# Kernel optimization log

Measured on AMD Instinct MI355X. Metric: run time of the kernel, lower is better.

The kernel has to match this reference:

```python
import jax, jax.numpy as jnp
import numpy as np
import math

L_LAYERS = 4
D = 768
H = 12
HD = D // H
S = 2048
BATCH = 1
V = 32000
R = 32
DFF = 3072
LORA_SCALE = 1.0 / R
EPS = 1e-6
NEG_INF = -1e9


def _alibi_slopes(n):
    def pow2(m):
        start = 2 ** (-2 ** (-(math.log2(m) - 3)))
        ratio = 2 ** (1.0 / m)
        return [start / ratio ** i for i in range(m)]
    if n <= 8:
        return [2 ** (-8.0 / n * (i + 1)) for i in range(n)]
    if math.log2(n).is_integer():
        return pow2(n)
    cp = 2 ** round(math.log2(n))
    base = pow2(cp)
    if n > cp:
        extra = []
        for _ in range(n - cp):
            r = base[-1] / base[-2] if len(base) > 1 else 0.5
            extra.append(base[-1] * r)
        return base + extra
    return base[:n]


def setup_inputs() -> dict:
    key = jax.random.key(0)
    ks = iter(jax.random.split(key, 24))
    def w(shape):
        return jax.random.normal(next(ks), shape, dtype=jnp.float32) * 0.02
    return {
        'input_ids': jax.random.randint(next(ks), (BATCH, S), 0, V),
        'emb': w((V, D)),
        'slopes': jnp.array(_alibi_slopes(H), dtype=jnp.float32),
        'ln1_g': jnp.ones((L_LAYERS, D), jnp.float32),
        'ln1_b': jnp.zeros((L_LAYERS, D), jnp.float32),
        'qkv_W': w((L_LAYERS, 3 * D, D)),
        'qkv_A': w((L_LAYERS, D, R)),
        'qkv_B': w((L_LAYERS, R, 3 * D)),
        'out_W': w((L_LAYERS, D, D)),
        'out_A': w((L_LAYERS, D, R)),
        'out_B': w((L_LAYERS, R, D)),
        'ln2_g': jnp.ones((L_LAYERS, D), jnp.float32),
        'ln2_b': jnp.zeros((L_LAYERS, D), jnp.float32),
        'fc1_W': w((L_LAYERS, 2 * DFF, D)),
        'fc1_A': w((L_LAYERS, D, R)),
        'fc1_B': w((L_LAYERS, R, 2 * DFF)),
        'fc2_W': w((L_LAYERS, D, DFF)),
        'fc2_A': w((L_LAYERS, DFF, R)),
        'fc2_B': w((L_LAYERS, R, D)),
        'ls1': 0.1 * jnp.ones((L_LAYERS, D), jnp.float32),
        'ls2': 0.1 * jnp.ones((L_LAYERS, D), jnp.float32),
        'lnf_g': jnp.ones((D,), jnp.float32),
        'lnf_b': jnp.zeros((D,), jnp.float32),
    }


def _ln(x, g, b):
    m = x.mean(-1, keepdims=True)
    v = jnp.mean((x - m) ** 2, -1, keepdims=True)
    return (x - m) * jax.lax.rsqrt(v + EPS) * g + b


def _lora(x, W, A, B):
    # base nn.Linear (weight [out,in], no bias) + low-rank adaptation
    return x @ W.T + (x @ A) @ B * LORA_SCALE


def _forward(input_ids, emb, slopes, ln1_g, ln1_b, qkv_W, qkv_A, qkv_B,
             out_W, out_A, out_B, ln2_g, ln2_b, fc1_W, fc1_A, fc1_B,
             fc2_W, fc2_A, fc2_B, ls1, ls2, lnf_g, lnf_b):
    bsz, s = input_ids.shape
    n_heads = slopes.shape[0]
    hd = emb.shape[1] // n_heads
    d = emb.shape[1]
    x = emb[input_ids]  # [B,S,D]

    # ALiBi bias + causal mask: [H,S,S]
    pos = jnp.arange(s)
    rel = pos[None, :] - pos[:, None]  # j - i, <= 0 in causal region
    bias = jnp.where(rel <= 0, slopes[:, None, None] * rel, NEG_INF)

    scale = 1.0 / math.sqrt(hd)
    n_layers = qkv_W.shape[0]
    for l in range(n_layers):
        # --- attention block ---
        h = _ln(x, ln1_g[l], ln1_b[l])
        qkv = _lora(h, qkv_W[l], qkv_A[l], qkv_B[l])  # [B,S,3D]
        qkv = qkv.reshape(bsz, s, 3, n_heads, hd)
        q = qkv[:, :, 0].transpose(0, 2, 1, 3)  # [B,H,S,hd]
        k = qkv[:, :, 1].transpose(0, 2, 1, 3)
        v = qkv[:, :, 2].transpose(0, 2, 1, 3)
        scores = jnp.einsum('bhid,bhjd->bhij', q, k) * scale + bias[None]
        wts = jax.nn.softmax(scores, axis=-1)
        ao = jnp.einsum('bhij,bhjd->bhid', wts, v)
        ao = ao.transpose(0, 2, 1, 3).reshape(bsz, s, d)
        ao = _lora(ao, out_W[l], out_A[l], out_B[l])
        x = x + ls1[l] * ao  # LayerScale, dropout=identity (eval)

        # --- SwiGLU FFN block ---
        h = _ln(x, ln2_g[l], ln2_b[l])
        hidden = _lora(h, fc1_W[l], fc1_A[l], fc1_B[l])  # [B,S,2*DFF]
        gated, activated = jnp.split(hidden, 2, axis=-1)
        ff = jax.nn.silu(gated) * activated
        ff = _lora(ff, fc2_W[l], fc2_A[l], fc2_B[l])
        x = x + ls2[l] * ff

    x = _ln(x, lnf_g, lnf_b)
    logits = x @ emb.T  # tied lm_head
    return logits


def reference(input_ids, emb, slopes, ln1_g, ln1_b, qkv_W, qkv_A, qkv_B,
              out_W, out_A, out_B, ln2_g, ln2_b, fc1_W, fc1_A, fc1_B,
              fc2_W, fc2_A, fc2_B, ls1, ls2, lnf_g, lnf_b):
    return _forward(input_ids, emb, slopes, ln1_g, ln1_b, qkv_W, qkv_A, qkv_B,
                    out_W, out_A, out_B, ln2_g, ln2_b, fc1_W, fc1_A, fc1_B,
                    fc2_W, fc2_A, fc2_B, ls1, ls2, lnf_g, lnf_b)
```

## Files before the change

kernel.cpp:

```cpp
#include <hip/hip_runtime.h>
#include <hip/hip_bf16.h>
#include <stdint.h>

#define S 2048
#define D 768
#define H 12
#define HD 64
#define V 32000
#define R 32
#define DFF 3072
#define NLAYERS 4
#define EPS 1e-6f

typedef __bf16 bf16;
typedef __bf16 bf16x4 __attribute__((ext_vector_type(4)));
typedef __bf16 bf16x8 __attribute__((ext_vector_type(8)));
typedef float f32x4 __attribute__((ext_vector_type(4)));

__device__ __forceinline__ int swz_logical(int nwg) {
    int id = blockIdx.x;
    int q = nwg >> 3;
    return (id & 7) * q + (id >> 3);
}

__global__ __launch_bounds__(256) void k_cvt(const float* __restrict__ in,
                                             bf16* __restrict__ out, long n) {
    long i = ((long)blockIdx.x * 256 + threadIdx.x) * 4;
    if (i >= n) return;
    float4 v = *(const float4*)(in + i);
    bf16x4 o;
    o.x = (bf16)v.x; o.y = (bf16)v.y; o.z = (bf16)v.z; o.w = (bf16)v.w;
    *(bf16x4*)(out + i) = o;
}

__global__ __launch_bounds__(256) void k_fold(const float* __restrict__ W,
                                              const float* __restrict__ A,
                                              const float* __restrict__ B,
                                              bf16* __restrict__ Wb,
                                              int N, int K) {
    __shared__ float As[256][33];
    int l = blockIdx.z;
    const float* Wl = W + (long)l * N * K;
    const float* Al = A + (long)l * K * R;
    const float* Bl = B + (long)l * R * N;
    bf16* Wbl = Wb + (long)l * N * K;
    int t = threadIdx.x;
    long k0 = (long)blockIdx.x * 256;
    int n0 = blockIdx.y * 8;
    const float* Ab = Al + k0 * R;
    #pragma unroll
    for (int i = 0; i < 32; ++i) {
        int idx = i * 256 + t;
        As[idx >> 5][idx & 31] = Ab[idx];
    }
    __syncthreads();
    long k = k0 + t;
    float acc[8];
    #pragma unroll
    for (int j = 0; j < 8; ++j) acc[j] = Wl[(long)(n0 + j) * K + k];
    for (int r = 0; r < R; ++r) {
        float a = As[t][r] * (1.0f / R);
        #pragma unroll
        for (int j = 0; j < 8; ++j)
            acc[j] = fmaf(a, Bl[(long)r * N + n0 + j], acc[j]);
    }
    #pragma unroll
    for (int j = 0; j < 8; ++j) Wbl[(long)(n0 + j) * K + k] = (bf16)acc[j];
}

__global__ void k_embed(const int* __restrict__ ids, const float* __restrict__ emb,
                        float* __restrict__ x) {
    int s = blockIdx.x;
    int row = ids[s];
    for (int d = threadIdx.x; d < D; d += blockDim.x)
        x[s * D + d] = emb[row * D + d];
}

__global__ __launch_bounds__(256) void k_ln_bf(const float* __restrict__ x,
                                               const float* __restrict__ g,
                                               const float* __restrict__ b,
                                               bf16* __restrict__ out) {
    int w = threadIdx.x >> 6, lane = threadIdx.x & 63;
    long s = (long)blockIdx.x * 4 + w;
    const float* xr = x + s * D;
    float4 v0 = *(const float4*)(xr + lane * 4);
    float4 v1 = *(const float4*)(xr + 256 + lane * 4);
    float4 v2 = *(const float4*)(xr + 512 + lane * 4);
    float sum = v0.x + v0.y + v0.z + v0.w + v1.x + v1.y + v1.z + v1.w
              + v2.x + v2.y + v2.z + v2.w;
    float sq = v0.x*v0.x + v0.y*v0.y + v0.z*v0.z + v0.w*v0.w
             + v1.x*v1.x + v1.y*v1.y + v1.z*v1.z + v1.w*v1.w
             + v2.x*v2.x + v2.y*v2.y + v2.z*v2.z + v2.w*v2.w;
    #pragma unroll
    for (int m = 1; m < 64; m <<= 1) {
        sum += __shfl_xor(sum, m);
        sq  += __shfl_xor(sq, m);
    }
    float mean = sum * (1.0f / D);
    float var  = sq * (1.0f / D) - mean * mean;
    float rs = rsqrtf(var + EPS);
    bf16* orow = out + s * D;
    #pragma unroll
    for (int j = 0; j < 3; ++j) {
        float4 v = (j == 0) ? v0 : (j == 1) ? v1 : v2;
        float4 gv = *(const float4*)(g + j * 256 + lane * 4);
        float4 bv = *(const float4*)(b + j * 256 + lane * 4);
        bf16x4 o;
        o[0] = (bf16)((v.x - mean) * rs * gv.x + bv.x);
        o[1] = (bf16)((v.y - mean) * rs * gv.y + bv.y);
        o[2] = (bf16)((v.z - mean) * rs * gv.z + bv.z);
        o[3] = (bf16)((v.w - mean) * rs * gv.w + bv.w);
        *(bf16x4*)(orow + j * 256 + lane * 4) = o;
    }
}

__device__ __forceinline__ void gload16(const bf16* g, bf16* l) {
    __builtin_amdgcn_global_load_lds(
        (const __attribute__((address_space(1))) void*)g,
        (__attribute__((address_space(3))) void*)l, 16, 0, 0);
}

__global__ __launch_bounds__(256) void k_gemm_lm(const bf16* __restrict__ X,
                                                 const bf16* __restrict__ W,
                                                 float* __restrict__ C,
                                                 int N, int K, int nwg) {
    __shared__ bf16 At[128 * 32];
    __shared__ bf16 Bt[128 * 32];
    int tid = threadIdx.x;
    int w = tid >> 6, lane = tid & 63;
    int logical = swz_logical(nwg);
    long m0 = (long)(logical & 15) * 128;
    long n0 = (long)(logical >> 4) * 128;
    int wr = (w >> 1) * 64, wc = (w & 1) * 64;
    int c0 = w, c1 = w + 4;
    int rA0 = c0 * 16 + (lane >> 2);
    int rA1 = c1 * 16 + (lane >> 2);
    int ck = (lane & 3) * 8;
    int fr = lane & 15;
    int fo = (lane >> 4) * 8;
    f32x4 acc[4][4] = {};
    for (int k0 = 0; k0 < K; k0 += 32) {
        gload16(X + (m0 + rA0) * K + k0 + ck, At + c0 * 512);
        gload16(X + (m0 + rA1) * K + k0 + ck, At + c1 * 512);
        gload16(W + (n0 + rA0) * K + k0 + ck, Bt + c0 * 512);
        gload16(W + (n0 + rA1) * K + k0 + ck, Bt + c1 * 512);
        __syncthreads();
        bf16x8 a[4], b[4];
        #pragma unroll
        for (int m = 0; m < 4; m++)
            a[m] = *(const bf16x8*)(At + (wr + m * 16 + fr) * 32 + fo);
        #pragma unroll
        for (int n = 0; n < 4; n++)
            b[n] = *(const bf16x8*)(Bt + (wc + n * 16 + fr) * 32 + fo);
        #pragma unroll
        for (int m = 0; m < 4; m++)
            #pragma unroll
            for (int n = 0; n < 4; n++)
                acc[m][n] = __builtin_amdgcn_mfma_f32_16x16x32_bf16(a[m], b[n], acc[m][n], 0, 0, 0);
        __syncthreads();
    }
    int cr = (lane >> 4) * 4, cc = lane & 15;
    #pragma unroll
    for (int m = 0; m < 4; m++)
        #pragma unroll
        for (int n = 0; n < 4; n++) {
            long col = n0 + wc + n * 16 + cc;
            #pragma unroll
            for (int r = 0; r < 4; r++) {
                long idx = (m0 + wr + m * 16 + cr + r) * N + col;
                C[idx] = acc[m][n][r];
            }
        }
}

template <int TAG>
__global__ __launch_bounds__(256) void k_gemm_small(const bf16* __restrict__ X,
                                                    const bf16* __restrict__ W,
                                                    float* __restrict__ C,
                                                    int N, int K,
                                                    const float* __restrict__ ls,
                                                    int nwg) {
    __shared__ bf16 At[64 * 64];
    __shared__ bf16 Bt[128 * 64];
    int tid = threadIdx.x;
    int w = tid >> 6, lane = tid & 63;
    int logical = swz_logical(nwg);
    long m0 = (long)(logical & 31) * 64;
    long n0 = (long)(logical >> 5) * 128;
    int wr = (w >> 1) * 32, wc = (w & 1) * 64;
    int fr = lane & 15;
    int g  = lane >> 4;
    f32x4 acc[2][4] = {};
    for (int k0 = 0; k0 < K; k0 += 64) {
        #pragma unroll
        for (int i = 0; i < 2; ++i) {
            int ci = tid + 256 * i;
            int r = ci >> 3, c = (ci & 7) ^ (r & 7);
            gload16(X + (m0 + r) * K + k0 + c * 8, At + ci * 8);
        }
        #pragma unroll
        for (int i = 0; i < 4; ++i) {
            int ci = tid + 256 * i;
            int r = ci >> 3, c = (ci & 7) ^ (r & 7);
            gload16(W + (n0 + r) * K + k0 + c * 8, Bt + ci * 8);
        }
        __syncthreads();
        #pragma unroll
        for (int kk = 0; kk < 2; ++kk) {
            bf16x8 a[2], b[4];
            #pragma unroll
            for (int m = 0; m < 2; m++) {
                int row = wr + m * 16 + fr;
                a[m] = *(const bf16x8*)(At + row * 64 + (((kk * 4 + g) ^ (row & 7)) * 8));
            }
            #pragma unroll
            for (int n = 0; n < 4; n++) {
                int row = wc + n * 16 + fr;
                b[n] = *(const bf16x8*)(Bt + row * 64 + (((kk * 4 + g) ^ (row & 7)) * 8));
            }
            #pragma unroll
            for (int m = 0; m < 2; m++)
                #pragma unroll
                for (int n = 0; n < 4; n++)
                    acc[m][n] = __builtin_amdgcn_mfma_f32_16x16x32_bf16(a[m], b[n], acc[m][n], 0, 0, 0);
        }
        __syncthreads();
    }
    int cr = (lane >> 4) * 4, cc = lane & 15;
    #pragma unroll
    for (int m = 0; m < 2; m++)
        #pragma unroll
        for (int n = 0; n < 4; n++) {
            long col = n0 + wc + n * 16 + cc;
            #pragma unroll
            for (int r = 0; r < 4; r++) {
                long idx = (m0 + wr + m * 16 + cr + r) * N + col;
                C[idx] = fmaf(ls[col], acc[m][n][r], C[idx]);
            }
        }
}

__global__ __launch_bounds__(256) void k_gemm_qkv(const bf16* __restrict__ X,
                                                  const bf16* __restrict__ W,
                                                  bf16* __restrict__ Qh,
                                                  bf16* __restrict__ Kh,
                                                  bf16* __restrict__ Vt,
                                                  int nwg) {
    const int K = D;
    __shared__ bf16 smem[128 * 136];
    bf16* At = smem;
    bf16* Bt = smem + 128 * 32;
    int tid = threadIdx.x;
    int w = tid >> 6, lane = tid & 63;
    int logical = swz_logical(nwg);
    long m0 = (long)(logical & 15) * 128;
    long n0 = (long)(logical >> 4) * 128;
    int wr = (w >> 1) * 64, wc = (w & 1) * 64;
    int c0 = w, c1 = w + 4;
    int rA0 = c0 * 16 + (lane >> 2);
    int rA1 = c1 * 16 + (lane >> 2);
    int ck = (lane & 3) * 8;
    int fr = lane & 15;
    int fo = (lane >> 4) * 8;
    f32x4 acc[4][4] = {};
    for (int k0 = 0; k0 < K; k0 += 32) {
        gload16(X + (m0 + rA0) * K + k0 + ck, At + c0 * 512);
        gload16(X + (m0 + rA1) * K + k0 + ck, At + c1 * 512);
        gload16(W + (n0 + rA0) * K + k0 + ck, Bt + c0 * 512);
        gload16(W + (n0 + rA1) * K + k0 + ck, Bt + c1 * 512);
        __syncthreads();
        bf16x8 a[4], b[4];
        #pragma unroll
        for (int m = 0; m < 4; m++)
            a[m] = *(const bf16x8*)(At + (wr + m * 16 + fr) * 32 + fo);
        #pragma unroll
        for (int n = 0; n < 4; n++)
            b[n] = *(const bf16x8*)(Bt + (wc + n * 16 + fr) * 32 + fo);
        #pragma unroll
        for (int m = 0; m < 4; m++)
            #pragma unroll
            for (int n = 0; n < 4; n++)
                acc[m][n] = __builtin_amdgcn_mfma_f32_16x16x32_bf16(a[m], b[n], acc[m][n], 0, 0, 0);
        __syncthreads();
    }
    int cr = (lane >> 4) * 4, cc = lane & 15;
    if (n0 < 1536) {
        float scale = (n0 < 768) ? 0.125f : 1.0f;
        bf16* dst = (n0 < 768) ? Qh : Kh;
        int base = (n0 < 768) ? (int)n0 : (int)n0 - 768;
        #pragma unroll
        for (int m = 0; m < 4; m++)
            #pragma unroll
            for (int n = 0; n < 4; n++)
                #pragma unroll
                for (int r = 0; r < 4; r++)
                    smem[(wr + m * 16 + cr + r) * 136 + wc + n * 16 + cc] =
                        (bf16)(acc[m][n][r] * scale);
        __syncthreads();
        #pragma unroll
        for (int i = 0; i < 8; ++i) {
            int c = tid + 256 * i;
            int srow = c >> 4, off = (c & 15) * 8;
            int hh = (base >> 6) + (off >> 6);
            int d0 = off & 63;
            bf16x8 vv = *(const bf16x8*)(smem + srow * 136 + off);
            *(bf16x8*)(dst + ((long)hh * S + m0 + srow) * HD + d0) = vv;
        }
    } else {
        int base = (int)n0 - 1536;
        #pragma unroll
        for (int m = 0; m < 4; m++)
            #pragma unroll
            for (int n = 0; n < 4; n++) {
                bf16x4 pv;
                #pragma unroll
                for (int r = 0; r < 4; ++r) pv[r] = (bf16)acc[m][n][r];
                *(bf16x4*)(smem + (wc + n * 16 + cc) * 136 + wr + m * 16 + cr) = pv;
            }
        __syncthreads();
        #pragma unroll
        for (int i = 0; i < 8; ++i) {
            int c = tid + 256 * i;
            int vcol = c >> 4, soff = (c & 15) * 8;
            bf16x8 vv = *(const bf16x8*)(smem + vcol * 136 + soff);
            *(bf16x8*)(Vt + (long)(base + vcol) * S + m0 + soff) = vv;
        }
    }
}

__global__ __launch_bounds__(256) void k_gemm_fc1(const bf16* __restrict__ X,
                                                  const bf16* __restrict__ W,
                                                  bf16* __restrict__ hb,
                                                  int nwg) {
    const int K = D;
    __shared__ bf16 At[128 * 32];
    __shared__ bf16 Bg[128 * 32];
    __shared__ bf16 Ba[128 * 32];
    int tid = threadIdx.x;
    int w = tid >> 6, lane = tid & 63;
    int logical = swz_logical(nwg);
    long m0 = (long)(logical & 15) * 128;
    long f0 = (long)(logical >> 4) * 128;
    int wr = (w >> 1) * 64, wc = (w & 1) * 64;
    int c0 = w, c1 = w + 4;
    int rA0 = c0 * 16 + (lane >> 2);
    int rA1 = c1 * 16 + (lane >> 2);
    int ck = (lane & 3) * 8;
    int fr = lane & 15;
    int fo = (lane >> 4) * 8;
    const bf16* Wg = W + f0 * K;
    const bf16* Wa = W + ((long)DFF + f0) * K;
    f32x4 accG[4][4] = {}, accA[4][4] = {};
    for (int k0 = 0; k0 < K; k0 += 32) {
        gload16(X + (m0 + rA0) * K + k0 + ck, At + c0 * 512);
        gload16(X + (m0 + rA1) * K + k0 + ck, At + c1 * 512);
        gload16(Wg + (long)rA0 * K + k0 + ck, Bg + c0 * 512);
        gload16(Wg + (long)rA1 * K + k0 + ck, Bg + c1 * 512);
        gload16(Wa + (long)rA0 * K + k0 + ck, Ba + c0 * 512);
        gload16(Wa + (long)rA1 * K + k0 + ck, Ba + c1 * 512);
        __syncthreads();
        bf16x8 a[4], bg[4], ba[4];
        #pragma unroll
        for (int m = 0; m < 4; m++)
            a[m] = *(const bf16x8*)(At + (wr + m * 16 + fr) * 32 + fo);
        #pragma unroll
        for (int n = 0; n < 4; n++) {
            bg[n] = *(const bf16x8*)(Bg + (wc + n * 16 + fr) * 32 + fo);
            ba[n] = *(const bf16x8*)(Ba + (wc + n * 16 + fr) * 32 + fo);
        }
        #pragma unroll
        for (int m = 0; m < 4; m++)
            #pragma unroll
            for (int n = 0; n < 4; n++) {
                accG[m][n] = __builtin_amdgcn_mfma_f32_16x16x32_bf16(a[m], bg[n], accG[m][n], 0, 0, 0);
                accA[m][n] = __builtin_amdgcn_mfma_f32_16x16x32_bf16(a[m], ba[n], accA[m][n], 0, 0, 0);
            }
        __syncthreads();
    }
    int cr = (lane >> 4) * 4, cc = lane & 15;
    #pragma unroll
    for (int m = 0; m < 4; m++)
        #pragma unroll
        for (int n = 0; n < 4; n++) {
            long col = f0 + wc + n * 16 + cc;
            #pragma unroll
            for (int r = 0; r < 4; r++) {
                long s = m0 + wr + m * 16 + cr + r;
                float gv = accG[m][n][r], av = accA[m][n][r];
                float sig = 1.0f / (1.0f + __expf(-gv));
                hb[s * DFF + col] = (bf16)(gv * sig * av);
            }
        }
}

__global__ __launch_bounds__(256) void k_attn_mfma(const bf16* __restrict__ Qh,
                                                   const bf16* __restrict__ Kh,
                                                   const bf16* __restrict__ Vt,
                                                   const float* __restrict__ slopes,
                                                   bf16* __restrict__ ao) {
    __shared__ bf16 Kl[128 * 64];
    __shared__ bf16 Vl[64 * 128];
    __shared__ bf16 Pl[4][16 * 136];
    int tid = threadIdx.x;
    int w = tid >> 6, lane = tid & 63;
    int fr = lane & 15, g = lane >> 4;
    int qb = gridDim.x - 1 - blockIdx.x;
    int q0 = qb * 64;
    int h = blockIdx.y;
    int ntiles = qb / 2 + 1;
    float slope = slopes[h];

    const bf16* qrow = Qh + ((long)h * S + q0 + w * 16 + fr) * HD;
    bf16x8 qf0 = *(const bf16x8*)(qrow + g * 8);
    bf16x8 qf1 = *(const bf16x8*)(qrow + 32 + g * 8);

    const bf16* Kg = Kh + (long)h * S * HD;
    const bf16* Vg = Vt + (long)h * HD * S;

    float m = -1e9f, l = 0.f;
    f32x4 o[4] = {};
    int qg = q0 + w * 16 + fr;

    for (int t = 0; t < ntiles; ++t) {
        int j0 = t * 128;
        __syncthreads();
        #pragma unroll
        for (int i = 0; i < 4; ++i) {
            int ci = tid + 256 * i;
            int r = ci >> 3, c = (ci & 7) ^ (r & 7);
            gload16(Kg + (long)(j0 + r) * HD + c * 8, Kl + ci * 8);
        }
        #pragma unroll
        for (int i = 0; i < 4; ++i) {
            int ci = tid + 256 * i;
            int rd = ci >> 4, cj = (ci & 15) ^ (rd & 7);
            gload16(Vg + (long)rd * S + j0 + cj * 8, Vl + ci * 8);
        }
        __syncthreads();

        f32x4 sc[8];
        __builtin_amdgcn_s_setprio(1);
        #pragma unroll
        for (int jt = 0; jt < 8; ++jt) {
            int jr = jt * 16 + fr;
            bf16x8 kf0 = *(const bf16x8*)(Kl + jr * 64 + ((g ^ (jr & 7)) * 8));
            bf16x8 kf1 = *(const bf16x8*)(Kl + jr * 64 + (((g + 4) ^ (jr & 7)) * 8));
            f32x4 z = {};
            z = __builtin_amdgcn_mfma_f32_16x16x32_bf16(kf0, qf0, z, 0, 0, 0);
            z = __builtin_amdgcn_mfma_f32_16x16x32_bf16(kf1, qf1, z, 0, 0, 0);
            sc[jt] = z;
        }
        __builtin_amdgcn_s_setprio(0);

        bool need_mask = (j0 + 127) > (q0 + w * 16);
        float mt = -1e9f;
        if (need_mask) {
            #pragma unroll
            for (int jt = 0; jt < 8; ++jt)
                #pragma unroll
                for (int r = 0; r < 4; ++r) {
                    int rel = (j0 + jt * 16 + g * 4 + r) - qg;
                    float v = (rel <= 0) ? fmaf(slope, (float)rel, sc[jt][r]) : -1e9f;
                    sc[jt][r] = v;
                    mt = fmaxf(mt, v);
                }
        } else {
            #pragma unroll
            for (int jt = 0; jt < 8; ++jt)
                #pragma unroll
                for (int r = 0; r < 4; ++r) {
                    int rel = (j0 + jt * 16 + g * 4 + r) - qg;
                    float v = fmaf(slope, (float)rel, sc[jt][r]);
                    sc[jt][r] = v;
                    mt = fmaxf(mt, v);
                }
        }
        mt = fmaxf(mt, __shfl_xor(mt, 16));
        mt = fmaxf(mt, __shfl_xor(mt, 32));
        float mnew = fmaxf(m, mt);
        float factor = __expf(m - mnew);
        float psum = 0.f;
        #pragma unroll
        for (int jt = 0; jt < 8; ++jt) {
            bf16x4 pb;
            #pragma unroll
            for (int r = 0; r < 4; ++r) {
                float p = __expf(sc[jt][r] - mnew);
                psum += p;
                pb[r] = (bf16)p;
            }
            *(bf16x4*)(&Pl[w][fr * 136 + jt * 16 + g * 4]) = pb;
        }
        psum += __shfl_xor(psum, 16);
        psum += __shfl_xor(psum, 32);
        l = l * factor + psum;
        m = mnew;
        #pragma unroll
        for (int dt = 0; dt < 4; ++dt)
            #pragma unroll
            for (int r = 0; r < 4; ++r) o[dt][r] *= factor;

        bf16x8 pf[4];
        #pragma unroll
        for (int ks = 0; ks < 4; ++ks)
            pf[ks] = *(const bf16x8*)(&Pl[w][fr * 136 + ks * 32 + g * 8]);
        __builtin_amdgcn_s_setprio(1);
        #pragma unroll
        for (int dt = 0; dt < 4; ++dt) {
            int dr = dt * 16 + fr;
            #pragma unroll
            for (int ks = 0; ks < 4; ++ks) {
                bf16x8 vf = *(const bf16x8*)(Vl + dr * 128 + (((ks * 4 + g) ^ (dr & 7)) * 8));
                o[dt] = __builtin_amdgcn_mfma_f32_16x16x32_bf16(vf, pf[ks], o[dt], 0, 0, 0);
            }
        }
        __builtin_amdgcn_s_setprio(0);
    }
    float inv = 1.0f / l;
    bf16* orow = ao + ((long)(q0 + w * 16 + fr)) * D + h * HD;
    #pragma unroll
    for (int dt = 0; dt < 4; ++dt) {
        bf16x4 ob;
        #pragma unroll
        for (int r = 0; r < 4; ++r) ob[r] = (bf16)(o[dt][r] * inv);
        *(bf16x4*)(orow + dt * 16 + g * 4) = ob;
    }
}

extern "C" void kernel_launch(void* const* d_in, const int* in_sizes, int n_in,
                              void* d_out, int out_size, void* d_ws, size_t ws_size,
                              hipStream_t stream) {
    const int*   ids    = (const int*)d_in[0];
    const float* emb    = (const float*)d_in[1];
    const float* slopes = (const float*)d_in[2];
    const float* ln1_g  = (const float*)d_in[3];
    const float* ln1_b  = (const float*)d_in[4];
    const float* qkv_W  = (const float*)d_in[5];
    const float* qkv_A  = (const float*)d_in[6];
    const float* qkv_B  = (const float*)d_in[7];
    const float* out_W  = (const float*)d_in[8];
    const float* out_A  = (const float*)d_in[9];
    const float* out_B  = (const float*)d_in[10];
    const float* ln2_g  = (const float*)d_in[11];
    const float* ln2_b  = (const float*)d_in[12];
    const float* fc1_W  = (const float*)d_in[13];
    const float* fc1_A  = (const float*)d_in[14];
    const float* fc1_B  = (const float*)d_in[15];
    const float* fc2_W  = (const float*)d_in[16];
    const float* fc2_A  = (const float*)d_in[17];
    const float* fc2_B  = (const float*)d_in[18];
    const float* ls1    = (const float*)d_in[19];
    const float* ls2    = (const float*)d_in[20];
    const float* lnf_g  = (const float*)d_in[21];
    const float* lnf_b  = (const float*)d_in[22];

    char* p = (char*)d_ws;
    float* x      = (float*)p;               p += (long)S * D * 4;
    bf16* h_bf    = (bf16*)p;                p += (long)S * D * 2;
    bf16* ao_bf   = (bf16*)p;                p += (long)S * D * 2;
    bf16* hid_bf  = (bf16*)p;                p += (long)S * DFF * 2;
    bf16* Qh      = (bf16*)p;                p += (long)H * S * HD * 2;
    bf16* Kh      = (bf16*)p;                p += (long)H * S * HD * 2;
    bf16* Vt      = (bf16*)p;                p += (long)H * HD * S * 2;
    bf16* emb_bf  = (bf16*)p;                p += (long)V * D * 2;
    bf16* qkvW_bf = (bf16*)p;                p += (long)NLAYERS * 3 * D * D * 2;
    bf16* outW_bf = (bf16*)p;                p += (long)NLAYERS * D * D * 2;
    bf16* fc1W_bf = (bf16*)p;                p += (long)NLAYERS * 2 * DFF * D * 2;
    bf16* fc2W_bf = (bf16*)p;                p += (long)NLAYERS * D * DFF * 2;

    k_fold<<<dim3(D / 256, 3 * D / 8, NLAYERS), 256, 0, stream>>>(qkv_W, qkv_A, qkv_B, qkvW_bf, 3 * D, D);
    k_fold<<<dim3(D / 256, D / 8, NLAYERS), 256, 0, stream>>>(out_W, out_A, out_B, outW_bf, D, D);
    k_fold<<<dim3(D / 256, 2 * DFF / 8, NLAYERS), 256, 0, stream>>>(fc1_W, fc1_A, fc1_B, fc1W_bf, 2 * DFF, D);
    k_fold<<<dim3(DFF / 256, D / 8, NLAYERS), 256, 0, stream>>>(fc2_W, fc2_A, fc2_B, fc2W_bf, D, DFF);
    {
        long n = (long)V * D;
        k_cvt<<<(n / 4 + 255) / 256, 256, 0, stream>>>(emb, emb_bf, n);
    }

    k_embed<<<S, 256, 0, stream>>>(ids, emb, x);

    const int NWG_QKV = (3 * D / 128) * 16;
    const int NWG_FC1 = (DFF / 128) * 16;
    const int NWG_SM  = (S / 64) * (D / 128);
    const int NWG_LM  = (V / 128) * 16;

    for (int l = 0; l < NLAYERS; l++) {
        k_ln_bf<<<S / 4, 256, 0, stream>>>(x, ln1_g + l * D, ln1_b + l * D, h_bf);
        k_gemm_qkv<<<NWG_QKV, 256, 0, stream>>>(h_bf, qkvW_bf + (long)l * 3 * D * D, Qh, Kh, Vt, NWG_QKV);
        k_attn_mfma<<<dim3(S / 64, H), 256, 0, stream>>>(Qh, Kh, Vt, slopes, ao_bf);
        k_gemm_small<1><<<NWG_SM, 256, 0, stream>>>(ao_bf, outW_bf + (long)l * D * D, x, D, D, ls1 + l * D, NWG_SM);

        k_ln_bf<<<S / 4, 256, 0, stream>>>(x, ln2_g + l * D, ln2_b + l * D, h_bf);
        k_gemm_fc1<<<NWG_FC1, 256, 0, stream>>>(h_bf, fc1W_bf + (long)l * 2 * DFF * D, hid_bf, NWG_FC1);
        k_gemm_small<2><<<NWG_SM, 256, 0, stream>>>(hid_bf, fc2W_bf + (long)l * D * DFF, x, D, DFF, ls2 + l * D, NWG_SM);
    }

    k_ln_bf<<<S / 4, 256, 0, stream>>>(x, lnf_g, lnf_b, h_bf);
    k_gemm_lm<<<NWG_LM, 256, 0, stream>>>(h_bf, emb_bf, (float*)d_out, V, D, NWG_LM);
}
```

Measured before the change: 1.230 ms.

## Retile QKV and FC1 GEMMs to 64x128 tiles with K=64 and XOR-swizzled LDS

The QKV and fused FC1 SwiGLU GEMMs switch from 128x128 tiles with K-step 32 to 64x128 tiles with K-step 64. Shared-memory tiles now use an XOR swizzle on 16-byte chunks to avoid bank conflicts. Launch grids double accordingly, giving more workgroups and fewer syncs per K loop, to improve occupancy and wave coverage across CUs. The trade-off is less A/B reuse per tile and more redundant weight loads, plus the V-transpose epilogue now uses a narrower staging stride.

```diff
diff --git a/kernel.cpp b/kernel.cpp
--- a/kernel.cpp
+++ b/kernel.cpp
@@ -247,40 +247,51 @@
                                                   bf16* __restrict__ Vt,
                                                   int nwg) {
     const int K = D;
-    __shared__ bf16 smem[128 * 136];
+    __shared__ bf16 smem[64 * 64 + 128 * 64];
     bf16* At = smem;
-    bf16* Bt = smem + 128 * 32;
+    bf16* Bt = smem + 64 * 64;
     int tid = threadIdx.x;
     int w = tid >> 6, lane = tid & 63;
     int logical = swz_logical(nwg);
-    long m0 = (long)(logical & 15) * 128;
-    long n0 = (long)(logical >> 4) * 128;
-    int wr = (w >> 1) * 64, wc = (w & 1) * 64;
-    int c0 = w, c1 = w + 4;
-    int rA0 = c0 * 16 + (lane >> 2);
-    int rA1 = c1 * 16 + (lane >> 2);
-    int ck = (lane & 3) * 8;
+    long m0 = (long)(logical & 31) * 64;
+    long n0 = (long)(logical >> 5) * 128;
+    int wr = (w >> 1) * 32, wc = (w & 1) * 64;
     int fr = lane & 15;
-    int fo = (lane >> 4) * 8;
-    f32x4 acc[4][4] = {};
-    for (int k0 = 0; k0 < K; k0 += 32) {
-        gload16(X + (m0 + rA0) * K + k0 + ck, At + c0 * 512);
-        gload16(X + (m0 + rA1) * K + k0 + ck, At + c1 * 512);
-        gload16(W + (n0 + rA0) * K + k0 + ck, Bt + c0 * 512);
-        gload16(W + (n0 + rA1) * K + k0 + ck, Bt + c1 * 512);
-        __syncthreads();
-        bf16x8 a[4], b[4];
-        #pragma unroll
-        for (int m = 0; m < 4; m++)
-            a[m] = *(const bf16x8*)(At + (wr + m * 16 + fr) * 32 + fo);
-        #pragma unroll
-        for (int n = 0; n < 4; n++)
-            b[n] = *(const bf16x8*)(Bt + (wc + n * 16 + fr) * 32 + fo);
-        #pragma unroll
-        for (int m = 0; m < 4; m++)
-            #pragma unroll
-            for (int n = 0; n < 4; n++)
-                acc[m][n] = __builtin_amdgcn_mfma_f32_16x16x32_bf16(a[m], b[n], acc[m][n], 0, 0, 0);
+    int g  = lane >> 4;
+    f32x4 acc[2][4] = {};
+    for (int k0 = 0; k0 < K; k0 += 64) {
+        #pragma unroll
+        for (int i = 0; i < 2; ++i) {
+            int ci = tid + 256 * i;
+            int r = ci >> 3, c = (ci & 7) ^ (r & 7);
+            gload16(X + (m0 + r) * K + k0 + c * 8, At + ci * 8);
+        }
+        #pragma unroll
+        for (int i = 0; i < 4; ++i) {
+            int ci = tid + 256 * i;
+            int r = ci >> 3, c = (ci & 7) ^ (r & 7);
+            gload16(W + (n0 + r) * K + k0 + c * 8, Bt + ci * 8);
+        }
+        __syncthreads();
+        #pragma unroll
+        for (int kk = 0; kk < 2; ++kk) {
+            bf16x8 a[2], b[4];
+            #pragma unroll
+            for (int m = 0; m < 2; m++) {
+                int row = wr + m * 16 + fr;
+                a[m] = *(const bf16x8*)(At + row * 64 + (((kk * 4 + g) ^ (row & 7)) * 8));
+            }
+            #pragma unroll
+            for (int n = 0; n < 4; n++) {
+                int row = wc + n * 16 + fr;
+                b[n] = *(const bf16x8*)(Bt + row * 64 + (((kk * 4 + g) ^ (row & 7)) * 8));
+            }
+            #pragma unroll
+            for (int m = 0; m < 2; m++)
+                #pragma unroll
+                for (int n = 0; n < 4; n++)
+                    acc[m][n] = __builtin_amdgcn_mfma_f32_16x16x32_bf16(a[m], b[n], acc[m][n], 0, 0, 0);
+        }
         __syncthreads();
     }
     int cr = (lane >> 4) * 4, cc = lane & 15;
@@ -289,7 +300,7 @@
         bf16* dst = (n0 < 768) ? Qh : Kh;
         int base = (n0 < 768) ? (int)n0 : (int)n0 - 768;
         #pragma unroll
-        for (int m = 0; m < 4; m++)
+        for (int m = 0; m < 2; m++)
             #pragma unroll
             for (int n = 0; n < 4; n++)
                 #pragma unroll
@@ -298,7 +309,7 @@
                         (bf16)(acc[m][n][r] * scale);
         __syncthreads();
         #pragma unroll
-        for (int i = 0; i < 8; ++i) {
+        for (int i = 0; i < 4; ++i) {
             int c = tid + 256 * i;
             int srow = c >> 4, off = (c & 15) * 8;
             int hh = (base >> 6) + (off >> 6);
@@ -309,20 +320,20 @@
     } else {
         int base = (int)n0 - 1536;
         #pragma unroll
-        for (int m = 0; m < 4; m++)
+        for (int m = 0; m < 2; m++)
             #pragma unroll
             for (int n = 0; n < 4; n++) {
                 bf16x4 pv;
                 #pragma unroll
                 for (int r = 0; r < 4; ++r) pv[r] = (bf16)acc[m][n][r];
-                *(bf16x4*)(smem + (wc + n * 16 + cc) * 136 + wr + m * 16 + cr) = pv;
-            }
-        __syncthreads();
-        #pragma unroll
-        for (int i = 0; i < 8; ++i) {
+                *(bf16x4*)(smem + (wc + n * 16 + cc) * 72 + wr + m * 16 + cr) = pv;
+            }
+        __syncthreads();
+        #pragma unroll
+        for (int i = 0; i < 4; ++i) {
             int c = tid + 256 * i;
-            int vcol = c >> 4, soff = (c & 15) * 8;
-            bf16x8 vv = *(const bf16x8*)(smem + vcol * 136 + soff);
+            int vcol = c >> 3, soff = (c & 7) * 8;
+            bf16x8 vv = *(const bf16x8*)(smem + vcol * 72 + soff);
             *(bf16x8*)(Vt + (long)(base + vcol) * S + m0 + soff) = vv;
         }
     }
@@ -333,53 +344,63 @@
                                                   bf16* __restrict__ hb,
                                                   int nwg) {
     const int K = D;
-    __shared__ bf16 At[128 * 32];
-    __shared__ bf16 Bg[128 * 32];
-    __shared__ bf16 Ba[128 * 32];
+    __shared__ bf16 At[64 * 64];
+    __shared__ bf16 Bg[128 * 64];
+    __shared__ bf16 Ba[128 * 64];
     int tid = threadIdx.x;
     int w = tid >> 6, lane = tid & 63;
     int logical = swz_logical(nwg);
-    long m0 = (long)(logical & 15) * 128;
-    long f0 = (long)(logical >> 4) * 128;
-    int wr = (w >> 1) * 64, wc = (w & 1) * 64;
-    int c0 = w, c1 = w + 4;
-    int rA0 = c0 * 16 + (lane >> 2);
-    int rA1 = c1 * 16 + (lane >> 2);
-    int ck = (lane & 3) * 8;
+    long m0 = (long)(logical & 31) * 64;
+    long f0 = (long)(logical >> 5) * 128;
+    int wr = (w >> 1) * 32, wc = (w & 1) * 64;
     int fr = lane & 15;
-    int fo = (lane >> 4) * 8;
+    int g  = lane >> 4;
     const bf16* Wg = W + f0 * K;
     const bf16* Wa = W + ((long)DFF + f0) * K;
-    f32x4 accG[4][4] = {}, accA[4][4] = {};
-    for (int k0 = 0; k0 < K; k0 += 32) {
-        gload16(X + (m0 + rA0) * K + k0 + ck, At + c0 * 512);
-        gload16(X + (m0 + rA1) * K + k0 + ck, At + c1 * 512);
-        gload16(Wg + (long)rA0 * K + k0 + ck, Bg + c0 * 512);
-        gload16(Wg + (long)rA1 * K + k0 + ck, Bg + c1 * 512);
-        gload16(Wa + (long)rA0 * K + k0 + ck, Ba + c0 * 512);
-        gload16(Wa + (long)rA1 * K + k0 + ck, Ba + c1 * 512);
-        __syncthreads();
-        bf16x8 a[4], bg[4], ba[4];
-        #pragma unroll
-        for (int m = 0; m < 4; m++)
-            a[m] = *(const bf16x8*)(At + (wr + m * 16 + fr) * 32 + fo);
-        #pragma unroll
-        for (int n = 0; n < 4; n++) {
-            bg[n] = *(const bf16x8*)(Bg + (wc + n * 16 + fr) * 32 + fo);
-            ba[n] = *(const bf16x8*)(Ba + (wc + n * 16 + fr) * 32 + fo);
-        }
-        #pragma unroll
-        for (int m = 0; m < 4; m++)
+    f32x4 accG[2][4] = {}, accA[2][4] = {};
+    for (int k0 = 0; k0 < K; k0 += 64) {
+        #pragma unroll
+        for (int i = 0; i < 2; ++i) {
+            int ci = tid + 256 * i;
+            int r = ci >> 3, c = (ci & 7) ^ (r & 7);
+            gload16(X + (m0 + r) * K + k0 + c * 8, At + ci * 8);
+        }
+        #pragma unroll
+        for (int i = 0; i < 4; ++i) {
+            int ci = tid + 256 * i;
+            int r = ci >> 3, c = (ci & 7) ^ (r & 7);
+            gload16(Wg + (long)r * K + k0 + c * 8, Bg + ci * 8);
+            gload16(Wa + (long)r * K + k0 + c * 8, Ba + ci * 8);
+        }
+        __syncthreads();
+        #pragma unroll
+        for (int kk = 0; kk < 2; ++kk) {
+            bf16x8 a[2], bg[4], ba[4];
+            #pragma unroll
+            for (int m = 0; m < 2; m++) {
+                int row = wr + m * 16 + fr;
+                a[m] = *(const bf16x8*)(At + row * 64 + (((kk * 4 + g) ^ (row & 7)) * 8));
+            }
             #pragma unroll
             for (int n = 0; n < 4; n++) {
-                accG[m][n] = __builtin_amdgcn_mfma_f32_16x16x32_bf16(a[m], bg[n], accG[m][n], 0, 0, 0);
-                accA[m][n] = __builtin_amdgcn_mfma_f32_16x16x32_bf16(a[m], ba[n], accA[m][n], 0, 0, 0);
-            }
+                int row = wc + n * 16 + fr;
+                int off = row * 64 + (((kk * 4 + g) ^ (row & 7)) * 8);
+                bg[n] = *(const bf16x8*)(Bg + off);
+                ba[n] = *(const bf16x8*)(Ba + off);
+            }
+            #pragma unroll
+            for (int m = 0; m < 2; m++)
+                #pragma unroll
+                for (int n = 0; n < 4; n++) {
+                    accG[m][n] = __builtin_amdgcn_mfma_f32_16x16x32_bf16(a[m], bg[n], accG[m][n], 0, 0, 0);
+                    accA[m][n] = __builtin_amdgcn_mfma_f32_16x16x32_bf16(a[m], ba[n], accA[m][n], 0, 0, 0);
+                }
+        }
         __syncthreads();
     }
     int cr = (lane >> 4) * 4, cc = lane & 15;
     #pragma unroll
-    for (int m = 0; m < 4; m++)
+    for (int m = 0; m < 2; m++)
         #pragma unroll
         for (int n = 0; n < 4; n++) {
             long col = f0 + wc + n * 16 + cc;
@@ -579,8 +600,8 @@
 
     k_embed<<<S, 256, 0, stream>>>(ids, emb, x);
 
-    const int NWG_QKV = (3 * D / 128) * 16;
-    const int NWG_FC1 = (DFF / 128) * 16;
+    const int NWG_QKV = (S / 64) * (3 * D / 128);
+    const int NWG_FC1 = (S / 64) * (DFF / 128);
     const int NWG_SM  = (S / 64) * (D / 128);
     const int NWG_LM  = (V / 128) * 16;
 
```

After: 1.100 ms. -10.5%, faster.
